# Performance work log

Measured on AMD Instinct MI355X. Metric: run time of the kernel, lower is better.

The kernel has to match this reference:

```python
import jax, jax.numpy as jnp
import numpy as np

T = 4096
STATE_DIM = 400
EMBED_DIM = 300
WIDTH_DIM = 20
HID = 150
GI_DIM = 2 * STATE_DIM + EMBED_DIM + WIDTH_DIM
BINS = (1, 2, 3, 4, 8, 16, 32, 64)
MAX_W = 10


def _dtoi(d):
    return sum(1 for b in BINS if d >= b)


def _mlp(x, W1, b1, W2, b2, W3, b3):
    h = jax.nn.relu(x @ W1 + b1)
    h = jax.nn.relu(h @ W2 + b2)
    return h @ W3 + b3


def setup_inputs() -> dict:
    key = jax.random.key(0)
    ks = jax.random.split(key, 16)
    s = 0.02
    return {
        "embeds": jax.random.normal(ks[0], (T, EMBED_DIM), jnp.float32),
        "states": jax.random.normal(ks[1], (T, STATE_DIM), jnp.float32),
        # attention Scorer (state_dim -> 150 -> 150 -> 1)
        "aW1": jax.random.normal(ks[2], (STATE_DIM, HID), jnp.float32) * s,
        "ab1": jnp.zeros((HID,), jnp.float32),
        "aW2": jax.random.normal(ks[3], (HID, HID), jnp.float32) * s,
        "ab2": jnp.zeros((HID,), jnp.float32),
        "aW3": jax.random.normal(ks[4], (HID, 1), jnp.float32) * s,
        "ab3": jnp.zeros((1,), jnp.float32),
        # width embedding table: len(BINS)+1 rows
        "width_table": jax.random.normal(ks[5], (len(BINS) + 1, WIDTH_DIM), jnp.float32) * s,
        # sm Scorer (gi_dim -> 150 -> 150 -> 1)
        "sW1": jax.random.normal(ks[6], (GI_DIM, HID), jnp.float32) * s,
        "sb1": jnp.zeros((HID,), jnp.float32),
        "sW2": jax.random.normal(ks[7], (HID, HID), jnp.float32) * s,
        "sb2": jnp.zeros((HID,), jnp.float32),
        "sW3": jax.random.normal(ks[8], (HID, 1), jnp.float32) * s,
        "sb3": jnp.zeros((1,), jnp.float32),
    }


def reference(embeds, states, aW1, ab1, aW2, ab2, aW3, ab3, width_table,
              sW1, sb1, sW2, sb2, sW3, sb3):
    t = states.shape[0]
    attn_scores = _mlp(states, aW1, ab1, aW2, ab2, aW3, ab3)[:, 0]  # [T]

    gs_parts, width_parts = [], []
    for n in range(1, MAX_W + 1):  # fixed, small window-size loop
        w = t - n + 1
        starts = jnp.arange(w)
        idx = starts[:, None] + jnp.arange(n)[None, :]        # [W, n]
        a = jax.nn.softmax(attn_scores[idx], axis=1)           # per-span softmax
        pooled = jnp.einsum('wn,wnd->wd', a, embeds[idx])      # [W, embed]
        g = jnp.concatenate([states[starts], states[starts + n - 1], pooled], axis=1)
        gs_parts.append(g)
        width_parts.append(width_table[_dtoi(n)][None, :].repeat(w, axis=0))

    gs = jnp.concatenate(gs_parts, axis=0)                     # [S, 2*state+embed]
    widths = jnp.concatenate(width_parts, axis=0)              # [S, width_dim]
    gs = jnp.concatenate([gs, widths], axis=1)                 # [S, gi_dim]
    sms = _mlp(gs, sW1, sb1, sW2, sb2, sW3, sb3)[:, 0]         # [S]
    return sms
```

## Files before the change

kernel.cpp:

```cpp
#include <hip/hip_runtime.h>
#include <hip/hip_bf16.h>

#define T_TOK 4096
#define HID   150
#define HPAD  160
#define NSPAN 40915
#define MAXW  10
#define NT    10

typedef __attribute__((ext_vector_type(8))) _Float16 f16x8;
typedef __attribute__((ext_vector_type(4))) _Float16 f16x4;
typedef __attribute__((ext_vector_type(4))) float    f32x4;

__global__ __launch_bounds__(256) void k_prep(
    const float* __restrict__ states, const float* __restrict__ embeds,
    const float* __restrict__ aW1, const float* __restrict__ sW1,
    const float* __restrict__ aW2, const float* __restrict__ sW2,
    const float* __restrict__ wt, const float* __restrict__ sb1,
    _Float16* __restrict__ Sf, _Float16* __restrict__ Ef,
    _Float16* __restrict__ fW1, _Float16* __restrict__ fA1,
    _Float16* __restrict__ fB1, _Float16* __restrict__ fE1,
    _Float16* __restrict__ fA2, _Float16* __restrict__ fW2,
    float* __restrict__ wc)
{
    const int b = blockIdx.x;
    const int w = threadIdx.x >> 6, l = threadIdx.x & 63;

    if (b < 1472) {
        const float* src; int lda, srcK, KT; _Float16* d; int tb;
        if (b < 832) { src = states; lda = 400; srcK = 400; KT = 13; d = Sf; tb = b * 4 + w; }
        else         { src = embeds; lda = 300; srcK = 300; KT = 10; d = Ef; tb = (b - 832) * 4 + w; }
        int mt = tb / KT;
        int m = mt * 16 + (l & 15);
        int kbase = (tb - mt * KT) * 32 + (l >> 4) * 8;
        const float* row = src + (size_t)m * lda;
        f16x8 hv;
#pragma unroll
        for (int e = 0; e < 8; e++) {
            int k = kbase + e;
            float f = (k < srcK) ? row[k] : 0.f;
            hv[e] = (_Float16)f;
        }
        *(f16x8*)(d + ((size_t)tb * 64 + l) * 8) = hv;
    } else if (b < 1620) {
        int tw = (b - 1472) * 4 + w;
        if (tw >= 590) return;
        const float* src; int srcK, off; _Float16* d;
        if      (tw < 130) { src = aW1;             srcK = 400; off = 0;   d = fW1; }
        else if (tw < 260) { src = sW1;             srcK = 400; off = 130; d = fA1; }
        else if (tw < 390) { src = sW1 + 400 * HID; srcK = 400; off = 260; d = fB1; }
        else if (tw < 490) { src = sW1 + 800 * HID; srcK = 300; off = 390; d = fE1; }
        else if (tw < 540) { src = aW2;             srcK = 150; off = 490; d = fA2; }
        else               { src = sW2;             srcK = 150; off = 540; d = fW2; }
        int tb = tw - off;
        int kt = tb / NT, nt = tb - kt * NT;
        int n = nt * 16 + (l & 15);
        int kbase = kt * 32 + (l >> 4) * 8;
        f16x8 hv;
#pragma unroll
        for (int e = 0; e < 8; e++) {
            int k = kbase + e;
            float f = (k < srcK && n < HID) ? src[(size_t)k * HID + n] : 0.f;
            hv[e] = (_Float16)f;
        }
        *(f16x8*)(d + ((size_t)tb * 64 + l) * 8) = hv;
    } else {
        int n = b - 1619;
        int c = threadIdx.x;
        if (c >= HPAD) return;
        float s = 0.f;
        if (c < HID) {
            const int dt[11] = {0, 1, 2, 3, 4, 4, 4, 4, 5, 5, 5};
            const float* ww = wt + dt[n] * 20;
            s = sb1[c];
#pragma unroll
            for (int j = 0; j < 20; j++) s = fmaf(ww[j], sW1[(1100 + j) * HID + c], s);
        }
        wc[(n - 1) * HPAD + c] = s;
    }
}

__global__ __launch_bounds__(256) void k_proj(
    const _Float16* __restrict__ Sf, const _Float16* __restrict__ Ef,
    const _Float16* __restrict__ fW1, const _Float16* __restrict__ fA1,
    const _Float16* __restrict__ fB1, const _Float16* __restrict__ fE1,
    const _Float16* __restrict__ fA2,
    const float* __restrict__ ab1, const float* __restrict__ ab2,
    const float* __restrict__ aW3, const float* __restrict__ ab3,
    _Float16* __restrict__ Abuf, _Float16* __restrict__ Bbuf,
    _Float16* __restrict__ Ebuf, float* __restrict__ scores)
{
    __shared__ alignas(16) _Float16 hh[5120];
    __shared__ float red[4][16];

    const _Float16 *Af_, *Bf_; int KT; _Float16* C = nullptr;
    switch (blockIdx.y) {
        case 0: Af_=Sf; Bf_=fW1; KT=13; break;
        case 1: Af_=Sf; Bf_=fA1; KT=13; C=Abuf; break;
        case 2: Af_=Sf; Bf_=fB1; KT=13; C=Bbuf; break;
        default:Af_=Ef; Bf_=fE1; KT=10; C=Ebuf; break;
    }
    const int w = threadIdx.x >> 6, l = threadIdx.x & 63;
    const int mtl = w >> 1;
    const int mt  = blockIdx.x * 2 + mtl;
    const int nh  = w & 1;
    const f16x8* pA = (const f16x8*)Af_;
    const f16x8* pB = (const f16x8*)Bf_;

    f32x4 acc[5];
#pragma unroll
    for (int c = 0; c < 5; c++) acc[c] = (f32x4){0.f, 0.f, 0.f, 0.f};

#pragma unroll 2
    for (int kt = 0; kt < KT; ++kt) {
        f16x8 a = pA[(size_t)(mt * KT + kt) * 64 + l];
#pragma unroll
        for (int c = 0; c < 5; c++) {
            f16x8 bv = pB[(size_t)(kt * NT + nh * 5 + c) * 64 + l];
            acc[c] = __builtin_amdgcn_mfma_f32_16x16x32_f16(a, bv, acc[c], 0, 0, 0);
        }
    }

    if (blockIdx.y != 0) {
        const int m0 = mt * 16;
#pragma unroll
        for (int c = 0; c < 5; c++) {
            int col = (nh * 5 + c) * 16 + (l & 15);
#pragma unroll
            for (int r = 0; r < 4; r++) {
                int row = m0 + (l >> 4) * 4 + r;
                C[(size_t)row * HPAD + col] = (_Float16)acc[c][r];
            }
        }
        return;
    }

    const int m15 = l & 15;
#pragma unroll
    for (int c = 0; c < 5; c++) {
        int u   = nh * 5 + c;
        int col = u * 16 + m15;
        float bb = (col < HID) ? ab1[col] : 0.f;
        int kt = u >> 1;
        int g  = (u & 1) * 2 + (m15 >> 3);
        int e  = m15 & 7;
#pragma unroll
        for (int r = 0; r < 4; r++) {
            int rloc = (l >> 4) * 4 + r;
            float v = fmaxf(acc[c][r] + bb, 0.f);
            hh[((mtl * 5 + kt) * 64 + g * 16 + rloc) * 8 + e] = (_Float16)v;
        }
    }
    __syncthreads();

    const f16x8* pH = (const f16x8*)hh;
    const f16x8* pB2 = (const f16x8*)fA2;
    f32x4 acc2[5];
#pragma unroll
    for (int c = 0; c < 5; c++) acc2[c] = (f32x4){0.f, 0.f, 0.f, 0.f};
#pragma unroll
    for (int kt = 0; kt < 5; ++kt) {
        f16x8 a = pH[(mtl * 5 + kt) * 64 + l];
#pragma unroll
        for (int c = 0; c < 5; c++) {
            f16x8 bv = pB2[(size_t)(kt * NT + nh * 5 + c) * 64 + l];
            acc2[c] = __builtin_amdgcn_mfma_f32_16x16x32_f16(a, bv, acc2[c], 0, 0, 0);
        }
    }
    float p[4] = {0.f, 0.f, 0.f, 0.f};
#pragma unroll
    for (int c = 0; c < 5; c++) {
        int col = (nh * 5 + c) * 16 + m15;
        float bb = (col < HID) ? ab2[col] : 0.f;
        float wv = (col < HID) ? aW3[col] : 0.f;
#pragma unroll
        for (int r = 0; r < 4; r++) {
            float v = fmaxf(acc2[c][r] + bb, 0.f);
            p[r] = fmaf(v, wv, p[r]);
        }
    }
#pragma unroll
    for (int off = 1; off < 16; off <<= 1)
#pragma unroll
        for (int r = 0; r < 4; r++) p[r] += __shfl_xor(p[r], off);
    if (m15 == 0)
#pragma unroll
        for (int r = 0; r < 4; r++) red[w][(l >> 4) * 4 + r] = p[r];
    __syncthreads();
    if (threadIdx.x < 32) {
        int ml = threadIdx.x;
        scores[blockIdx.x * 32 + ml] =
            red[(ml >> 4) * 2 + 0][ml & 15] + red[(ml >> 4) * 2 + 1][ml & 15] + ab3[0];
    }
}

__global__ __launch_bounds__(256) void k_spanfinal(
    const float* __restrict__ scores, const _Float16* __restrict__ Abuf,
    const _Float16* __restrict__ Bbuf, const _Float16* __restrict__ Ebuf,
    const float* __restrict__ wc,
    const _Float16* __restrict__ fW2,
    const float* __restrict__ sb2, const float* __restrict__ sW3,
    const float* __restrict__ sb3, float* __restrict__ out)
{
    __shared__ alignas(16) _Float16 hh[5120];
    __shared__ float wg[32][10];
    __shared__ int   stI[32], nnI[32];
    __shared__ float red[4][16];

    const int tid = threadIdx.x;
    const int s0  = blockIdx.x * 32;

    if (tid < 32) {
        int span = s0 + tid;
        int n = 1, start = 0;
        if (span < NSPAN) {
            int base = 0;
#pragma unroll
            for (int i = 1; i <= MAXW; i++) {
                int ww = T_TOK - i + 1;
                if (span < base + ww) { n = i; break; }
                base += ww;
            }
            start = span - base;
        }
        float sc[MAXW]; float mx = -1e30f;
#pragma unroll
        for (int i = 0; i < MAXW; i++) {
            sc[i] = (i < n) ? scores[start + i] : -1e30f;
            mx = fmaxf(mx, sc[i]);
        }
        float ssum = 0.f;
#pragma unroll
        for (int i = 0; i < MAXW; i++) { sc[i] = __expf(sc[i] - mx); ssum += sc[i]; }
        float inv = 1.f / ssum;
#pragma unroll
        for (int i = 0; i < MAXW; i++) wg[tid][i] = (i < n) ? sc[i] * inv : 0.f;
        stI[tid] = start;
        nnI[tid] = n;
    }
    __syncthreads();

#pragma unroll
    for (int it = 0; it < 5; ++it) {
        int task = it * 256 + tid;
        int sl = task / 40;
        int q  = task - sl * 40;
        int start = stI[sl], n = nnI[sl];
        int d0 = q * 4;
        float v0 = 0.f, v1 = 0.f, v2 = 0.f, v3 = 0.f;
        if (d0 < HID) {
            int endr = start + n - 1;
            f16x4 a4 = *(const f16x4*)(Abuf + (size_t)start * HPAD + d0);
            f16x4 b4 = *(const f16x4*)(Bbuf + (size_t)endr * HPAD + d0);
            float4 w4 = *(const float4*)(wc + (n - 1) * HPAD + d0);
            v0 = (float)a4[0] + (float)b4[0] + w4.x;
            v1 = (float)a4[1] + (float)b4[1] + w4.y;
            v2 = (float)a4[2] + (float)b4[2] + w4.z;
            v3 = (float)a4[3] + (float)b4[3] + w4.w;
            for (int i = 0; i < n; i++) {
                f16x4 e4 = *(const f16x4*)(Ebuf + (size_t)(start + i) * HPAD + d0);
                float a = wg[sl][i];
                v0 = fmaf(a, (float)e4[0], v0); v1 = fmaf(a, (float)e4[1], v1);
                v2 = fmaf(a, (float)e4[2], v2); v3 = fmaf(a, (float)e4[3], v3);
            }
            v0 = fmaxf(v0, 0.f); v1 = fmaxf(v1, 0.f);
            v2 = fmaxf(v2, 0.f); v3 = fmaxf(v3, 0.f);
        }
        int mtl = sl >> 4, sm = sl & 15;
        int kt = q >> 3, gg = (q >> 1) & 3, e0 = (q & 1) * 4;
        int slot = ((mtl * 5 + kt) * 64 + gg * 16 + sm) * 8 + e0;
        f16x4 hv;
        hv[0] = (_Float16)v0; hv[1] = (_Float16)v1;
        hv[2] = (_Float16)v2; hv[3] = (_Float16)v3;
        *(f16x4*)(hh + slot) = hv;
    }
    __syncthreads();

    const int w = tid >> 6, l = tid & 63;
    const int mtl = w >> 1, nh = w & 1;
    const int m15 = l & 15;
    const f16x8* pH = (const f16x8*)hh;
    const f16x8* pB = (const f16x8*)fW2;
    f32x4 acc[5];
#pragma unroll
    for (int c = 0; c < 5; c++) acc[c] = (f32x4){0.f, 0.f, 0.f, 0.f};
#pragma unroll
    for (int kt = 0; kt < 5; ++kt) {
        f16x8 a = pH[(mtl * 5 + kt) * 64 + l];
#pragma unroll
        for (int c = 0; c < 5; c++) {
            f16x8 bv = pB[(size_t)(kt * NT + nh * 5 + c) * 64 + l];
            acc[c] = __builtin_amdgcn_mfma_f32_16x16x32_f16(a, bv, acc[c], 0, 0, 0);
        }
    }
    float p[4] = {0.f, 0.f, 0.f, 0.f};
#pragma unroll
    for (int c = 0; c < 5; c++) {
        int col = (nh * 5 + c) * 16 + m15;
        float bb = (col < HID) ? sb2[col] : 0.f;
        float wv = (col < HID) ? sW3[col] : 0.f;
#pragma unroll
        for (int r = 0; r < 4; r++) {
            float v = fmaxf(acc[c][r] + bb, 0.f);
            p[r] = fmaf(v, wv, p[r]);
        }
    }
#pragma unroll
    for (int off = 1; off < 16; off <<= 1)
#pragma unroll
        for (int r = 0; r < 4; r++) p[r] += __shfl_xor(p[r], off);
    if (m15 == 0)
#pragma unroll
        for (int r = 0; r < 4; r++) red[w][(l >> 4) * 4 + r] = p[r];
    __syncthreads();
    if (tid < 32) {
        int row = s0 + tid;
        if (row < NSPAN)
            out[row] = red[(tid >> 4) * 2 + 0][tid & 15] +
                       red[(tid >> 4) * 2 + 1][tid & 15] + sb3[0];
    }
}

extern "C" void kernel_launch(void* const* d_in, const int* in_sizes, int n_in,
                              void* d_out, int out_size, void* d_ws, size_t ws_size,
                              hipStream_t stream) {
    const float* embeds = (const float*)d_in[0];
    const float* states = (const float*)d_in[1];
    const float* aW1 = (const float*)d_in[2];
    const float* ab1 = (const float*)d_in[3];
    const float* aW2 = (const float*)d_in[4];
    const float* ab2 = (const float*)d_in[5];
    const float* aW3 = (const float*)d_in[6];
    const float* ab3 = (const float*)d_in[7];
    const float* wt  = (const float*)d_in[8];
    const float* sW1 = (const float*)d_in[9];
    const float* sb1 = (const float*)d_in[10];
    const float* sW2 = (const float*)d_in[11];
    const float* sb2 = (const float*)d_in[12];
    const float* sW3 = (const float*)d_in[13];
    const float* sb3 = (const float*)d_in[14];
    float* out = (float*)d_out;

    char* W = (char*)d_ws;
    _Float16* Abuf = (_Float16*)(W + 0);
    _Float16* Bbuf = (_Float16*)(W + 1310720);
    _Float16* Ebuf = (_Float16*)(W + 2621440);
    float* scores  = (float*)(W + 3932160);
    float* wcbuf   = (float*)(W + 3948544);
    _Float16* Sf   = (_Float16*)(W + 3954944);
    _Float16* Ef   = (_Float16*)(W + 7362816);
    _Float16* fW1  = (_Float16*)(W + 9984256);
    _Float16* fA1  = (_Float16*)(W + 10117376);
    _Float16* fB1  = (_Float16*)(W + 10250496);
    _Float16* fE1  = (_Float16*)(W + 10383616);
    _Float16* fA2  = (_Float16*)(W + 10486016);
    _Float16* fW2  = (_Float16*)(W + 10537216);

    k_prep<<<1630, 256, 0, stream>>>(states, embeds, aW1, sW1, aW2, sW2, wt, sb1,
        Sf, Ef, fW1, fA1, fB1, fE1, fA2, fW2, wcbuf);
    k_proj<<<dim3(128, 4), 256, 0, stream>>>(Sf, Ef, fW1, fA1, fB1, fE1, fA2,
        ab1, ab2, aW3, ab3, Abuf, Bbuf, Ebuf, scores);
    k_spanfinal<<<1279, 256, 0, stream>>>(scores, Abuf, Bbuf, Ebuf, wcbuf,
        fW2, sb2, sW3, sb3, out);
}
```

Measured before the change: 41.10 us.

## Fuse fp32-to-fp16 activation conversion into projection GEMM and widen span gather

Drops the separate pass in k_prep that converted states and embeds into fp16 MFMA-tiled buffers. k_proj now loads the fp32 rows directly with float4 reads and converts them in registers before each MFMA, which removes a large global write and reread. The span-final gather also moves from 4-wide to 8-wide fp16 vectors, cutting its task count and the per-lane index math. The cost is that states rows are now read and converted by three y-blocks instead of once, and the A-operand loads are strided row accesses rather than prepacked tiles.

```diff
diff --git a/kernel.cpp b/kernel.cpp
--- a/kernel.cpp
+++ b/kernel.cpp
@@ -13,11 +13,9 @@
 typedef __attribute__((ext_vector_type(4))) float    f32x4;
 
 __global__ __launch_bounds__(256) void k_prep(
-    const float* __restrict__ states, const float* __restrict__ embeds,
     const float* __restrict__ aW1, const float* __restrict__ sW1,
     const float* __restrict__ aW2, const float* __restrict__ sW2,
     const float* __restrict__ wt, const float* __restrict__ sb1,
-    _Float16* __restrict__ Sf, _Float16* __restrict__ Ef,
     _Float16* __restrict__ fW1, _Float16* __restrict__ fA1,
     _Float16* __restrict__ fB1, _Float16* __restrict__ fE1,
     _Float16* __restrict__ fA2, _Float16* __restrict__ fW2,
@@ -26,24 +24,8 @@
     const int b = blockIdx.x;
     const int w = threadIdx.x >> 6, l = threadIdx.x & 63;
 
-    if (b < 1472) {
-        const float* src; int lda, srcK, KT; _Float16* d; int tb;
-        if (b < 832) { src = states; lda = 400; srcK = 400; KT = 13; d = Sf; tb = b * 4 + w; }
-        else         { src = embeds; lda = 300; srcK = 300; KT = 10; d = Ef; tb = (b - 832) * 4 + w; }
-        int mt = tb / KT;
-        int m = mt * 16 + (l & 15);
-        int kbase = (tb - mt * KT) * 32 + (l >> 4) * 8;
-        const float* row = src + (size_t)m * lda;
-        f16x8 hv;
-#pragma unroll
-        for (int e = 0; e < 8; e++) {
-            int k = kbase + e;
-            float f = (k < srcK) ? row[k] : 0.f;
-            hv[e] = (_Float16)f;
-        }
-        *(f16x8*)(d + ((size_t)tb * 64 + l) * 8) = hv;
-    } else if (b < 1620) {
-        int tw = (b - 1472) * 4 + w;
+    if (b < 148) {
+        int tw = b * 4 + w;
         if (tw >= 590) return;
         const float* src; int srcK, off; _Float16* d;
         if      (tw < 130) { src = aW1;             srcK = 400; off = 0;   d = fW1; }
@@ -65,7 +47,7 @@
         }
         *(f16x8*)(d + ((size_t)tb * 64 + l) * 8) = hv;
     } else {
-        int n = b - 1619;
+        int n = b - 147;
         int c = threadIdx.x;
         if (c >= HPAD) return;
         float s = 0.f;
@@ -81,7 +63,7 @@
 }
 
 __global__ __launch_bounds__(256) void k_proj(
-    const _Float16* __restrict__ Sf, const _Float16* __restrict__ Ef,
+    const float* __restrict__ states, const float* __restrict__ embeds,
     const _Float16* __restrict__ fW1, const _Float16* __restrict__ fA1,
     const _Float16* __restrict__ fB1, const _Float16* __restrict__ fE1,
     const _Float16* __restrict__ fA2,
@@ -93,19 +75,21 @@
     __shared__ alignas(16) _Float16 hh[5120];
     __shared__ float red[4][16];
 
-    const _Float16 *Af_, *Bf_; int KT; _Float16* C = nullptr;
+    const float* Asrc; int lda, srcK, KT; const _Float16* Bf; _Float16* C = nullptr;
     switch (blockIdx.y) {
-        case 0: Af_=Sf; Bf_=fW1; KT=13; break;
-        case 1: Af_=Sf; Bf_=fA1; KT=13; C=Abuf; break;
-        case 2: Af_=Sf; Bf_=fB1; KT=13; C=Bbuf; break;
-        default:Af_=Ef; Bf_=fE1; KT=10; C=Ebuf; break;
+        case 0: Asrc = states; lda = 400; srcK = 400; KT = 13; Bf = fW1; break;
+        case 1: Asrc = states; lda = 400; srcK = 400; KT = 13; Bf = fA1; C = Abuf; break;
+        case 2: Asrc = states; lda = 400; srcK = 400; KT = 13; Bf = fB1; C = Bbuf; break;
+        default:Asrc = embeds; lda = 300; srcK = 300; KT = 10; Bf = fE1; C = Ebuf; break;
     }
     const int w = threadIdx.x >> 6, l = threadIdx.x & 63;
     const int mtl = w >> 1;
     const int mt  = blockIdx.x * 2 + mtl;
     const int nh  = w & 1;
-    const f16x8* pA = (const f16x8*)Af_;
-    const f16x8* pB = (const f16x8*)Bf_;
+    const int m15 = l & 15;
+    const int koff = (l >> 4) * 8;
+    const float* arow = Asrc + (size_t)(mt * 16 + m15) * lda;
+    const f16x8* pB = (const f16x8*)Bf;
 
     f32x4 acc[5];
 #pragma unroll
@@ -113,7 +97,20 @@
 
 #pragma unroll 2
     for (int kt = 0; kt < KT; ++kt) {
-        f16x8 a = pA[(size_t)(mt * KT + kt) * 64 + l];
+        const int kbase = kt * 32 + koff;
+        f16x8 a;
+        if (kbase + 8 <= srcK) {
+            float4 v0 = *(const float4*)(arow + kbase);
+            float4 v1 = *(const float4*)(arow + kbase + 4);
+            a[0] = (_Float16)v0.x; a[1] = (_Float16)v0.y;
+            a[2] = (_Float16)v0.z; a[3] = (_Float16)v0.w;
+            a[4] = (_Float16)v1.x; a[5] = (_Float16)v1.y;
+            a[6] = (_Float16)v1.z; a[7] = (_Float16)v1.w;
+        } else {
+#pragma unroll
+            for (int e = 0; e < 8; e++)
+                a[e] = (_Float16)((kbase + e < srcK) ? arow[kbase + e] : 0.f);
+        }
 #pragma unroll
         for (int c = 0; c < 5; c++) {
             f16x8 bv = pB[(size_t)(kt * NT + nh * 5 + c) * 64 + l];
@@ -125,7 +122,7 @@
         const int m0 = mt * 16;
 #pragma unroll
         for (int c = 0; c < 5; c++) {
-            int col = (nh * 5 + c) * 16 + (l & 15);
+            int col = (nh * 5 + c) * 16 + m15;
 #pragma unroll
             for (int r = 0; r < 4; r++) {
                 int row = m0 + (l >> 4) * 4 + r;
@@ -135,7 +132,6 @@
         return;
     }
 
-    const int m15 = l & 15;
 #pragma unroll
     for (int c = 0; c < 5; c++) {
         int u   = nh * 5 + c;
@@ -241,38 +237,31 @@
     __syncthreads();
 
 #pragma unroll
-    for (int it = 0; it < 5; ++it) {
+    for (int it = 0; it < 3; ++it) {
         int task = it * 256 + tid;
-        int sl = task / 40;
-        int q  = task - sl * 40;
+        if (task >= 640) break;
+        int sl = task / 20;
+        int q  = task - sl * 20;
         int start = stI[sl], n = nnI[sl];
-        int d0 = q * 4;
-        float v0 = 0.f, v1 = 0.f, v2 = 0.f, v3 = 0.f;
-        if (d0 < HID) {
-            int endr = start + n - 1;
-            f16x4 a4 = *(const f16x4*)(Abuf + (size_t)start * HPAD + d0);
-            f16x4 b4 = *(const f16x4*)(Bbuf + (size_t)endr * HPAD + d0);
-            float4 w4 = *(const float4*)(wc + (n - 1) * HPAD + d0);
-            v0 = (float)a4[0] + (float)b4[0] + w4.x;
-            v1 = (float)a4[1] + (float)b4[1] + w4.y;
-            v2 = (float)a4[2] + (float)b4[2] + w4.z;
-            v3 = (float)a4[3] + (float)b4[3] + w4.w;
-            for (int i = 0; i < n; i++) {
-                f16x4 e4 = *(const f16x4*)(Ebuf + (size_t)(start + i) * HPAD + d0);
-                float a = wg[sl][i];
-                v0 = fmaf(a, (float)e4[0], v0); v1 = fmaf(a, (float)e4[1], v1);
-                v2 = fmaf(a, (float)e4[2], v2); v3 = fmaf(a, (float)e4[3], v3);
-            }
-            v0 = fmaxf(v0, 0.f); v1 = fmaxf(v1, 0.f);
-            v2 = fmaxf(v2, 0.f); v3 = fmaxf(v3, 0.f);
-        }
+        int d0 = q * 8;
+        f16x8 a8 = *(const f16x8*)(Abuf + (size_t)start * HPAD + d0);
+        f16x8 b8 = *(const f16x8*)(Bbuf + (size_t)(start + n - 1) * HPAD + d0);
+        const float* wr = wc + (n - 1) * HPAD + d0;
+        float v[8];
+#pragma unroll
+        for (int e = 0; e < 8; e++) v[e] = (float)a8[e] + (float)b8[e] + wr[e];
+        for (int i = 0; i < n; i++) {
+            f16x8 e8 = *(const f16x8*)(Ebuf + (size_t)(start + i) * HPAD + d0);
+            float aa = wg[sl][i];
+#pragma unroll
+            for (int e = 0; e < 8; e++) v[e] = fmaf(aa, (float)e8[e], v[e]);
+        }
+        f16x8 hv;
+#pragma unroll
+        for (int e = 0; e < 8; e++) hv[e] = (_Float16)fmaxf(v[e], 0.f);
         int mtl = sl >> 4, sm = sl & 15;
-        int kt = q >> 3, gg = (q >> 1) & 3, e0 = (q & 1) * 4;
-        int slot = ((mtl * 5 + kt) * 64 + gg * 16 + sm) * 8 + e0;
-        f16x4 hv;
-        hv[0] = (_Float16)v0; hv[1] = (_Float16)v1;
-        hv[2] = (_Float16)v2; hv[3] = (_Float16)v3;
-        *(f16x4*)(hh + slot) = hv;
+        int kt = q >> 2, gg = q & 3;
+        *(f16x8*)(hh + ((mtl * 5 + kt) * 64 + gg * 16 + sm) * 8) = hv;
     }
     __syncthreads();
 
@@ -347,19 +336,17 @@
     _Float16* Ebuf = (_Float16*)(W + 2621440);
     float* scores  = (float*)(W + 3932160);
     float* wcbuf   = (float*)(W + 3948544);
-    _Float16* Sf   = (_Float16*)(W + 3954944);
-    _Float16* Ef   = (_Float16*)(W + 7362816);
-    _Float16* fW1  = (_Float16*)(W + 9984256);
-    _Float16* fA1  = (_Float16*)(W + 10117376);
-    _Float16* fB1  = (_Float16*)(W + 10250496);
-    _Float16* fE1  = (_Float16*)(W + 10383616);
-    _Float16* fA2  = (_Float16*)(W + 10486016);
-    _Float16* fW2  = (_Float16*)(W + 10537216);
-
-    k_prep<<<1630, 256, 0, stream>>>(states, embeds, aW1, sW1, aW2, sW2, wt, sb1,
-        Sf, Ef, fW1, fA1, fB1, fE1, fA2, fW2, wcbuf);
-    k_proj<<<dim3(128, 4), 256, 0, stream>>>(Sf, Ef, fW1, fA1, fB1, fE1, fA2,
-        ab1, ab2, aW3, ab3, Abuf, Bbuf, Ebuf, scores);
+    _Float16* fW1  = (_Float16*)(W + 3954944);
+    _Float16* fA1  = (_Float16*)(W + 4088064);
+    _Float16* fB1  = (_Float16*)(W + 4221184);
+    _Float16* fE1  = (_Float16*)(W + 4354304);
+    _Float16* fA2  = (_Float16*)(W + 4456704);
+    _Float16* fW2  = (_Float16*)(W + 4507904);
+
+    k_prep<<<158, 256, 0, stream>>>(aW1, sW1, aW2, sW2, wt, sb1,
+                                    fW1, fA1, fB1, fE1, fA2, fW2, wcbuf);
+    k_proj<<<dim3(128, 4), 256, 0, stream>>>(states, embeds,
+        fW1, fA1, fB1, fE1, fA2, ab1, ab2, aW3, ab3, Abuf, Bbuf, Ebuf, scores);
     k_spanfinal<<<1279, 256, 0, stream>>>(scores, Abuf, Bbuf, Ebuf, wcbuf,
         fW2, sb2, sW3, sb3, out);
 }
```

Result: faster. 39.49 us (-3.9%).
